# Performance work log

Measured on AMD Instinct MI355X. Metric: run time of the kernel, lower is better.

The kernel has to match this reference:

```python
import jax, jax.numpy as jnp
import numpy as np

B, C, T = 64, 1, 262144
NUM_BANDS = 6
# (min, max) for each of the 18 normalized control params: 6 bands x (gain_dB, cutoff_Hz, Q)
PARAM_RANGES = np.array([
    [-24.0, 24.0], [20.0, 200.0], [0.1, 10.0],      # low shelf
    [-24.0, 24.0], [200.0, 2000.0], [0.1, 10.0],    # band 1
    [-24.0, 24.0], [200.0, 2000.0], [0.1, 10.0],    # band 2
    [-24.0, 24.0], [2000.0, 8000.0], [0.1, 10.0],   # band 3
    [-24.0, 24.0], [4000.0, 12000.0], [0.1, 10.0],  # band 4
    [-24.0, 24.0], [4000.0, 12000.0], [0.1, 10.0],  # high shelf
], dtype=np.float32)
FILTER_TYPES = ["low_shelf", "peaking", "peaking", "peaking", "peaking", "high_shelf"]


def biquad_coeffs(gain_dB, cutoff, q, sr, ftype):
    # Audio-EQ-cookbook biquad coefficients; all inputs shape (B,)
    A = 10.0 ** (gain_dB / 40.0)
    w0 = 2.0 * jnp.pi * (cutoff / sr)
    alpha = jnp.sin(w0) / (2.0 * q)
    c = jnp.cos(w0)
    sA = jnp.sqrt(A)
    if ftype == "low_shelf":
        b0 = A * ((A + 1) - (A - 1) * c + 2 * sA * alpha)
        b1 = 2 * A * ((A - 1) - (A + 1) * c)
        b2 = A * ((A + 1) - (A - 1) * c - 2 * sA * alpha)
        a0 = (A + 1) + (A - 1) * c + 2 * sA * alpha
        a1 = -2 * ((A - 1) + (A + 1) * c)
        a2 = (A + 1) + (A - 1) * c - 2 * sA * alpha
    elif ftype == "high_shelf":
        b0 = A * ((A + 1) + (A - 1) * c + 2 * sA * alpha)
        b1 = -2 * A * ((A - 1) + (A + 1) * c)
        b2 = A * ((A + 1) + (A - 1) * c - 2 * sA * alpha)
        a0 = (A + 1) - (A - 1) * c + 2 * sA * alpha
        a1 = 2 * ((A - 1) - (A + 1) * c)
        a2 = (A + 1) - (A - 1) * c - 2 * sA * alpha
    else:  # peaking
        b0 = 1 + alpha * A
        b1 = -2 * c
        b2 = 1 - alpha * A
        a0 = 1 + alpha / A
        a1 = -2 * c
        a2 = 1 - alpha / A
    bcoef = jnp.stack([b0, b1, b2], axis=-1) / a0[..., None]  # (B, 3)
    acoef = jnp.stack([a0, a1, a2], axis=-1) / a0[..., None]  # (B, 3)
    return bcoef, acoef


def cascade_biquads(x, bcoefs, acoefs):
    # x: (N, T); bcoefs/acoefs: (6, N, 3). Fused cascade of 6 biquads,
    # direct form II transposed, single scan over time.
    def step(state, xt):  # state: (6, N, 2); xt: (N,)
        v = xt
        new_states = []
        for k in range(NUM_BANDS):
            bk, ak = bcoefs[k], acoefs[k]
            s1, s2 = state[k, :, 0], state[k, :, 1]
            y = bk[:, 0] * v + s1
            ns1 = bk[:, 1] * v - ak[:, 1] * y + s2
            ns2 = bk[:, 2] * v - ak[:, 2] * y
            new_states.append(jnp.stack([ns1, ns2], axis=-1))
            v = y
        return jnp.stack(new_states, axis=0), v
    init = jnp.zeros((NUM_BANDS, x.shape[0], 2), dtype=x.dtype)
    _, y = jax.lax.scan(step, init, x.T)  # y: (T, N)
    return y.T


def setup_inputs() -> dict:
    key = jax.random.key(0)
    k1, k2, k3 = jax.random.split(key, 3)
    x = jax.random.normal(k1, (B, C, T), dtype=jnp.float32) * 0.1
    p = jax.random.normal(k2, (B, 22), dtype=jnp.float32)
    W = jax.random.normal(k3, (18, 22), dtype=jnp.float32) * (1.0 / np.sqrt(22.0))
    b = jnp.zeros((18,), dtype=jnp.float32)
    return {"x": x, "p": p, "W": W, "b": b, "sample_rate": 24000}


def reference(x, p, W, b, sample_rate):
    bs, chs, s = x.shape
    sr = jnp.float32(sample_rate)
    # control path: linear + sigmoid -> 18 normalized params in [0, 1]
    pn = jax.nn.sigmoid(p @ W.T + b)  # (bs, 18)
    lo = jnp.asarray(PARAM_RANGES[:, 0])
    hi = jnp.asarray(PARAM_RANGES[:, 1])
    params = pn * (hi - lo) + lo  # denormalized, (bs, 18)
    bcoefs, acoefs = [], []
    for k, ftype in enumerate(FILTER_TYPES):
        g, f, q = params[:, 3 * k], params[:, 3 * k + 1], params[:, 3 * k + 2]
        bk, ak = biquad_coeffs(g, f, q, sr, ftype)
        bcoefs.append(bk)
        acoefs.append(ak)
    bcoefs = jnp.stack(bcoefs, axis=0)  # (6, bs, 3)
    acoefs = jnp.stack(acoefs, axis=0)
    # share each item's EQ across its channels
    bcoefs = jnp.repeat(bcoefs, chs, axis=1)  # (6, bs*chs, 3)
    acoefs = jnp.repeat(acoefs, chs, axis=1)
    y = cascade_biquads(x.reshape(bs * chs, s), bcoefs, acoefs)
    return y.reshape(bs, chs, s)
```

## Files before the change

### kernel.cpp

```cpp
#include <hip/hip_runtime.h>
#include <math.h>

#define NB    64
#define NT    262144
#define CH    64
#define NCK   (NT/CH)
#define NBANDS 6

#define COEF_OFF 0
#define MAT_OFF  4096
#define T_OFF    (MAT_OFF + NB*1728)
#define V_OFF    (T_OFF + NB*64*12)

struct Coef { float b0, b1, b2, a1, a2; };

__device__ __forceinline__ float rfl(float x) {
  return __int_as_float(__builtin_amdgcn_readfirstlane(__float_as_int(x)));
}

__device__ __forceinline__ float cascade_step(float v, float s[12], const Coef cf[NBANDS]) {
#pragma unroll
  for (int k = 0; k < NBANDS; ++k) {
    float s1 = s[2*k], s2 = s[2*k+1];
    float y   = fmaf(cf[k].b0, v, s1);
    float ns1 = fmaf(cf[k].b1, v, fmaf(-cf[k].a1, y, s2));
    float ns2 = fmaf(cf[k].b2, v, -cf[k].a2 * y);
    s[2*k]   = ns1;
    s[2*k+1] = ns2;
    v = y;
  }
  return v;
}

__device__ __forceinline__ void load_coefs(const float* ws, int batch, Coef cf[NBANDS]) {
  const float* c = ws + COEF_OFF + batch*30;
#pragma unroll
  for (int k = 0; k < NBANDS; ++k) {
    cf[k].b0 = rfl(c[5*k+0]); cf[k].b1 = rfl(c[5*k+1]); cf[k].b2 = rfl(c[5*k+2]);
    cf[k].a1 = rfl(c[5*k+3]); cf[k].a2 = rfl(c[5*k+4]);
  }
}

__global__ __launch_bounds__(64) void k_prep(const float* __restrict__ p, const float* __restrict__ W,
                                             const float* __restrict__ bias, const int* __restrict__ srp,
                                             float* __restrict__ ws) {
  __shared__ float prmS[18];
  __shared__ float cfS[30];
  __shared__ float M0[144], M1[144];
  int b = blockIdx.x, tid = threadIdx.x;
  const float lo[18] = {-24.f,20.f,0.1f,  -24.f,200.f,0.1f,  -24.f,200.f,0.1f,
                        -24.f,2000.f,0.1f, -24.f,4000.f,0.1f, -24.f,4000.f,0.1f};
  const float hi[18] = { 24.f,200.f,10.f,  24.f,2000.f,10.f,  24.f,2000.f,10.f,
                         24.f,8000.f,10.f, 24.f,12000.f,10.f, 24.f,12000.f,10.f};
  if (tid < 18) {
    float acc = bias[tid];
    for (int j = 0; j < 22; ++j) acc = fmaf(W[tid*22+j], p[b*22+j], acc);
    float sg = 1.f / (1.f + expf(-acc));
    prmS[tid] = sg * (hi[tid] - lo[tid]) + lo[tid];
  }
  __syncthreads();
  if (tid < 6) {
    int k = tid;
    float g = prmS[3*k], f = prmS[3*k+1], q = prmS[3*k+2];
    float sr = (float)srp[0];
    float A  = powf(10.f, g * (1.f/40.f));
    float w0 = 6.28318530717958647692f * (f / sr);
    float al = sinf(w0) / (2.f*q);
    float c  = cosf(w0);
    float sA = sqrtf(A);
    float b0,b1,b2,a0,a1,a2;
    if (k == 0) {
      b0 = A*((A+1.f) - (A-1.f)*c + 2.f*sA*al);
      b1 = 2.f*A*((A-1.f) - (A+1.f)*c);
      b2 = A*((A+1.f) - (A-1.f)*c - 2.f*sA*al);
      a0 = (A+1.f) + (A-1.f)*c + 2.f*sA*al;
      a1 = -2.f*((A-1.f) + (A+1.f)*c);
      a2 = (A+1.f) + (A-1.f)*c - 2.f*sA*al;
    } else if (k == 5) {
      b0 = A*((A+1.f) + (A-1.f)*c + 2.f*sA*al);
      b1 = -2.f*A*((A-1.f) + (A+1.f)*c);
      b2 = A*((A+1.f) + (A-1.f)*c - 2.f*sA*al);
      a0 = (A+1.f) - (A-1.f)*c + 2.f*sA*al;
      a1 = 2.f*((A-1.f) - (A+1.f)*c);
      a2 = (A+1.f) - (A-1.f)*c - 2.f*sA*al;
    } else {
      b0 = 1.f + al*A;
      b1 = -2.f*c;
      b2 = 1.f - al*A;
      a0 = 1.f + al/A;
      a1 = -2.f*c;
      a2 = 1.f - al/A;
    }
    float inv = 1.f/a0;
    float* cws = ws + COEF_OFF + b*30;
    cws[5*k+0] = cfS[5*k+0] = b0*inv;
    cws[5*k+1] = cfS[5*k+1] = b1*inv;
    cws[5*k+2] = cfS[5*k+2] = b2*inv;
    cws[5*k+3] = cfS[5*k+3] = a1*inv;
    cws[5*k+4] = cfS[5*k+4] = a2*inv;
  }
  __syncthreads();

  Coef cf[NBANDS];
#pragma unroll
  for (int k = 0; k < NBANDS; ++k) {
    cf[k].b0 = cfS[5*k+0]; cf[k].b1 = cfS[5*k+1]; cf[k].b2 = cfS[5*k+2];
    cf[k].a1 = cfS[5*k+3]; cf[k].a2 = cfS[5*k+4];
  }
  if (tid < 12) {
    float s[12];
#pragma unroll
    for (int r = 0; r < 12; ++r) s[r] = (r == tid) ? 1.f : 0.f;
    cascade_step(0.f, s, cf);
#pragma unroll
    for (int r = 0; r < 12; ++r) M0[r*12 + tid] = s[r];
  }
  __syncthreads();

  float w[12];
#pragma unroll
  for (int r = 0; r < 12; ++r) w[r] = 0.f;
  cascade_step(1.f, w, cf);
  int e63 = 63 - tid;

  float* S = M0; float* D = M1;
  float* mout = ws + MAT_OFF + (size_t)b*1728;
  for (int q = 0; q < 6; ++q) {
    if ((e63 >> q) & 1) {
      float t[12];
#pragma unroll
      for (int r = 0; r < 12; ++r) {
        float acc = 0.f;
#pragma unroll
        for (int k = 0; k < 12; ++k) acc = fmaf(S[r*12+k], w[k], acc);
        t[r] = acc;
      }
#pragma unroll
      for (int r = 0; r < 12; ++r) w[r] = t[r];
    }
    for (int e = tid; e < 144; e += 64) {
      int r = e/12, c = e%12;
      float acc = 0.f;
#pragma unroll
      for (int k = 0; k < 12; ++k) acc = fmaf(S[r*12+k], S[k*12+c], acc);
      D[e] = acc;
    }
    __syncthreads();
    float* t = S; S = D; D = t;
  }
  {
    float* vout = ws + V_OFF + (size_t)b*768;
#pragma unroll
    for (int r = 0; r < 12; ++r) vout[tid*12 + r] = w[r];
  }
  for (int e = tid; e < 144; e += 64) mout[e] = S[e];
  for (int l = 1; l < 12; ++l) {
    for (int e = tid; e < 144; e += 64) {
      int r = e/12, c = e%12;
      float acc = 0.f;
#pragma unroll
      for (int k = 0; k < 12; ++k) acc = fmaf(S[r*12+k], S[k*12+c], acc);
      D[e] = acc;
    }
    __syncthreads();
    float* t = S; S = D; D = t;
    for (int e = tid; e < 144; e += 64) mout[l*144 + e] = S[e];
  }
}

__global__ __launch_bounds__(256, 4) void k_totals(const float* __restrict__ x,
                                                   float* __restrict__ ws) {
  __shared__ float KM[6][144];
  int tid = threadIdx.x, wib = tid >> 6, lane = tid & 63;
  int gw = blockIdx.x*4 + wib;
  int batch = gw >> 6, wv = gw & 63;
  int batch_b = blockIdx.x >> 4;

  const float* mb = ws + MAT_OFF + (size_t)batch_b*1728;
  for (int e = tid; e < 864; e += 256) KM[e/144][e%144] = mb[e];
  __syncthreads();

  const float4* x4 = (const float4*)x;
  size_t gbase4 = (size_t)batch*65536 + (size_t)wv*1024 + (size_t)lane*16;
  const float* Vb = ws + V_OFF + (size_t)batch_b*768;

  float4 xv[16];
#pragma unroll
  for (int k = 0; k < 16; ++k) xv[k] = x4[gbase4 + k];

  float s[12];
#pragma unroll
  for (int r = 0; r < 12; ++r) s[r] = 0.f;
#pragma unroll
  for (int k = 0; k < 16; ++k) {
    const float* vr = Vb + k*48;
#pragma unroll
    for (int r = 0; r < 12; ++r) {
      float acc = s[r];
      acc = fmaf(vr[r],      xv[k].x, acc);
      acc = fmaf(vr[12 + r], xv[k].y, acc);
      acc = fmaf(vr[24 + r], xv[k].z, acc);
      acc = fmaf(vr[36 + r], xv[k].w, acc);
      s[r] = acc;
    }
  }

#pragma unroll
  for (int l = 0; l < 6; ++l) {
    const int pd = 1 << l;
    float nb[12];
#pragma unroll
    for (int r = 0; r < 12; ++r) nb[r] = __shfl_up(s[r], pd);
    if (lane >= pd) {
#pragma unroll
      for (int r = 0; r < 12; ++r) {
        float acc = s[r];
#pragma unroll
        for (int c = 0; c < 12; ++c) acc = fmaf(KM[l][r*12+c], nb[c], acc);
        s[r] = acc;
      }
    }
  }

  if (lane == 63) {
    float4* tp = (float4*)(ws + T_OFF + ((size_t)batch*64 + wv)*12);
    tp[0] = make_float4(s[0], s[1], s[2],  s[3]);
    tp[1] = make_float4(s[4], s[5], s[6],  s[7]);
    tp[2] = make_float4(s[8], s[9], s[10], s[11]);
  }
}

__global__ __launch_bounds__(256, 4) void k_replay(const float* __restrict__ x,
                                                   const float* __restrict__ ws,
                                                   float* __restrict__ out) {
  __shared__ float KM[12][144];
  __shared__ float4 sbuf[4][256];
  int tid = threadIdx.x, wib = tid >> 6, lane = tid & 63;
  int gw = blockIdx.x*4 + wib;
  int batch = gw >> 6, wv = gw & 63;
  int batch_b = blockIdx.x >> 4;

  const float* mb = ws + MAT_OFF + (size_t)batch_b*1728;
  for (int e = tid; e < 1728; e += 256) KM[e/144][e%144] = mb[e];

  Coef cf[NBANDS];
  load_coefs(ws, batch, cf);
  __syncthreads();

  const float4* x4 = (const float4*)x;
  float4* out4 = (float4*)out;
  size_t wbase4 = (size_t)batch*65536 + (size_t)wv*1024;
  size_t gbase4 = wbase4 + (size_t)lane*16;
  const float* Vb = ws + V_OFF + (size_t)batch_b*768;

  float4 xv[16];
#pragma unroll
  for (int k = 0; k < 16; ++k) xv[k] = x4[gbase4 + k];

  float s[12];
#pragma unroll
  for (int r = 0; r < 12; ++r) s[r] = 0.f;
#pragma unroll
  for (int k = 0; k < 16; ++k) {
    const float* vr = Vb + k*48;
#pragma unroll
    for (int r = 0; r < 12; ++r) {
      float acc = s[r];
      acc = fmaf(vr[r],      xv[k].x, acc);
      acc = fmaf(vr[12 + r], xv[k].y, acc);
      acc = fmaf(vr[24 + r], xv[k].z, acc);
      acc = fmaf(vr[36 + r], xv[k].w, acc);
      s[r] = acc;
    }
  }

#pragma unroll
  for (int l = 0; l < 6; ++l) {
    const int pd = 1 << l;
    float nb[12];
#pragma unroll
    for (int r = 0; r < 12; ++r) nb[r] = __shfl_up(s[r], pd);
    if (lane >= pd) {
#pragma unroll
      for (int r = 0; r < 12; ++r) {
        float acc = s[r];
#pragma unroll
        for (int c = 0; c < 12; ++c) acc = fmaf(KM[l][r*12+c], nb[c], acc);
        s[r] = acc;
      }
    }
  }

  float ex[12];
#pragma unroll
  for (int r = 0; r < 12; ++r) ex[r] = __shfl_up(s[r], 1);
  if (lane == 0) {
#pragma unroll
    for (int r = 0; r < 12; ++r) ex[r] = 0.f;
  }

  const float4* tp = (const float4*)(ws + T_OFF + ((size_t)batch*64 + lane)*12);
  float4 t0 = tp[0], t1 = tp[1], t2 = tp[2];
  float sc[12] = {t0.x,t0.y,t0.z,t0.w, t1.x,t1.y,t1.z,t1.w, t2.x,t2.y,t2.z,t2.w};
#pragma unroll
  for (int l = 0; l < 6; ++l) {
    const int pd = 1 << l;
    float nb[12];
#pragma unroll
    for (int r = 0; r < 12; ++r) nb[r] = __shfl_up(sc[r], pd);
    if (lane >= pd) {
#pragma unroll
      for (int r = 0; r < 12; ++r) {
        float acc = sc[r];
#pragma unroll
        for (int c = 0; c < 12; ++c) acc = fmaf(KM[6+l][r*12+c], nb[c], acc);
        sc[r] = acc;
      }
    }
  }

  int bsrc = (wv == 0) ? 0 : (wv - 1);
  float pre[12];
#pragma unroll
  for (int r = 0; r < 12; ++r) pre[r] = __shfl(sc[r], bsrc);
  if (wv == 0) {
#pragma unroll
    for (int r = 0; r < 12; ++r) pre[r] = 0.f;
  }

  float R[12];
#pragma unroll
  for (int r = 0; r < 12; ++r) R[r] = pre[r];
#pragma unroll
  for (int l = 0; l < 6; ++l) {
    float t[12];
#pragma unroll
    for (int r = 0; r < 12; ++r) {
      float acc = 0.f;
#pragma unroll
      for (int c = 0; c < 12; ++c) acc = fmaf(KM[l][r*12+c], R[c], acc);
      t[r] = acc;
    }
    bool sel = (lane >> l) & 1;
#pragma unroll
    for (int r = 0; r < 12; ++r) R[r] = sel ? t[r] : R[r];
  }

  float st[12];
#pragma unroll
  for (int r = 0; r < 12; ++r) st[r] = ex[r] + R[r];

  int r2 = lane >> 2, c2 = lane & 3;
  float4* bp = sbuf[wib];
#pragma unroll
  for (int q = 0; q < 4; ++q) {
#pragma unroll
    for (int t = 0; t < 4; ++t) {
      float4 xvv = xv[q*4 + t];
      float4 yv;
      yv.x = cascade_step(xvv.x, st, cf);
      yv.y = cascade_step(xvv.y, st, cf);
      yv.z = cascade_step(xvv.z, st, cf);
      yv.w = cascade_step(xvv.w, st, cf);
      bp[t*64 + lane] = yv;
    }
    asm volatile("s_waitcnt lgkmcnt(0)" ::: "memory");
#pragma unroll
    for (int j = 0; j < 4; ++j) {
      float4 w = bp[c2*64 + j*16 + r2];
      out4[wbase4 + (size_t)(j*16 + r2)*16 + q*4 + c2] = w;
    }
    asm volatile("s_waitcnt lgkmcnt(0)" ::: "memory");
  }
}

extern "C" void kernel_launch(void* const* d_in, const int* in_sizes, int n_in,
                              void* d_out, int out_size, void* d_ws, size_t ws_size,
                              hipStream_t stream) {
  const float* x    = (const float*)d_in[0];
  const float* p    = (const float*)d_in[1];
  const float* W    = (const float*)d_in[2];
  const float* bias = (const float*)d_in[3];
  const int*   sr   = (const int*)d_in[4];
  float* ws  = (float*)d_ws;
  float* out = (float*)d_out;

  int passBlocks = (NB * NCK) / 256;
  hipLaunchKernelGGL(k_prep,   dim3(NB),         dim3(64),  0, stream, p, W, bias, sr, ws);
  hipLaunchKernelGGL(k_totals, dim3(passBlocks), dim3(256), 0, stream, x, ws);
  hipLaunchKernelGGL(k_replay, dim3(passBlocks), dim3(256), 0, stream, x, ws, out);
}
```

Baseline: 111.8 us.

## Fuse totals and replay passes into one single-pass decoupled-lookback scan kernel

Replaces the two-pass scheme (a totals kernel, then a replay kernel that re-reads x) with one kernel. Each block takes an atomic ticket, computes its segment aggregate, publishes it with a release flag, and waits on the preceding segments' flags before combining them with precomputed matrix powers. This removes one full read of the input and one kernel launch. In exchange it adds spin-waiting on flags, extra matrix-power precompute in k_prep, more shared memory per block, and a lower occupancy bound.

After: 164.5 us. 1.47x slower.

```diff
diff --git a/kernel.cpp b/kernel.cpp
--- a/kernel.cpp
+++ b/kernel.cpp
@@ -3,14 +3,17 @@
 
 #define NB    64
 #define NT    262144
-#define CH    64
-#define NCK   (NT/CH)
 #define NBANDS 6
+#define SEGS  16
+#define SEGLEN 16384
 
 #define COEF_OFF 0
 #define MAT_OFF  4096
-#define T_OFF    (MAT_OFF + NB*1728)
-#define V_OFF    (T_OFF + NB*64*12)
+#define V_OFF    (MAT_OFF + NB*1728)
+#define PW_OFF   (V_OFF + NB*768)
+#define AGG_OFF  (PW_OFF + NB*2304)
+#define FLAG_OFF (AGG_OFF + NB*192)
+#define TICKET_OFF (FLAG_OFF + NB*16)
 
 struct Coef { float b0, b1, b2, a1, a2; };
 
@@ -46,8 +49,12 @@
                                              float* __restrict__ ws) {
   __shared__ float prmS[18];
   __shared__ float cfS[30];
-  __shared__ float M0[144], M1[144];
+  __shared__ float M0[144], M1[144], M2[144];
   int b = blockIdx.x, tid = threadIdx.x;
+
+  if (tid < SEGS) ((int*)ws)[FLAG_OFF + b*SEGS + tid] = 0;
+  if (b == 0 && tid == 0) ((int*)ws)[TICKET_OFF] = 0;
+
   const float lo[18] = {-24.f,20.f,0.1f,  -24.f,200.f,0.1f,  -24.f,200.f,0.1f,
                         -24.f,2000.f,0.1f, -24.f,4000.f,0.1f, -24.f,4000.f,0.1f};
   const float hi[18] = { 24.f,200.f,10.f,  24.f,2000.f,10.f,  24.f,2000.f,10.f,
@@ -166,27 +173,63 @@
     float* t = S; S = D; D = t;
     for (int e = tid; e < 144; e += 64) mout[l*144 + e] = S[e];
   }
-}
-
-__global__ __launch_bounds__(256, 4) void k_totals(const float* __restrict__ x,
-                                                   float* __restrict__ ws) {
-  __shared__ float KM[6][144];
-  int tid = threadIdx.x, wib = tid >> 6, lane = tid & 63;
-  int gw = blockIdx.x*4 + wib;
-  int batch = gw >> 6, wv = gw & 63;
-  int batch_b = blockIdx.x >> 4;
-
-  const float* mb = ws + MAT_OFF + (size_t)batch_b*1728;
-  for (int e = tid; e < 864; e += 256) KM[e/144][e%144] = mb[e];
-  __syncthreads();
+
+  __syncthreads();
+  for (int e = tid; e < 144; e += 64) M0[e] = mout[8*144 + e];
+  for (int e = tid; e < 144; e += 64) M1[e] = (e/12 == e%12) ? 1.f : 0.f;
+  __syncthreads();
+  float* Pc = M1; float* Pd = M2;
+  float* pout = ws + PW_OFF + (size_t)b*2304;
+  for (int e = tid; e < 144; e += 64) pout[e] = Pc[e];
+  for (int k = 1; k < 16; ++k) {
+    for (int e = tid; e < 144; e += 64) {
+      int r = e/12, c = e%12;
+      float acc = 0.f;
+#pragma unroll
+      for (int j = 0; j < 12; ++j) acc = fmaf(Pc[r*12+j], M0[j*12+c], acc);
+      Pd[e] = acc;
+    }
+    __syncthreads();
+    float* t = Pc; Pc = Pd; Pd = t;
+    for (int e = tid; e < 144; e += 64) pout[k*144 + e] = Pc[e];
+  }
+}
+
+__global__ __launch_bounds__(256, 2) void k_scan(const float* __restrict__ x,
+                                                 float* __restrict__ ws,
+                                                 float* __restrict__ out) {
+  __shared__ float KM[8][144];
+  __shared__ float PS[16][144];
+  __shared__ float Tsh[4][12];
+  __shared__ float S0sh[12];
+  __shared__ float4 buf[4][256];
+  __shared__ int vbidS;
+
+  int tid = threadIdx.x, w = tid >> 6, lane = tid & 63;
+
+  if (tid == 0) vbidS = atomicAdd((int*)ws + TICKET_OFF, 1);
+  __syncthreads();
+  int vbid = vbidS;
+  int batch = vbid >> 4, seg = vbid & (SEGS-1);
 
   const float4* x4 = (const float4*)x;
-  size_t gbase4 = (size_t)batch*65536 + (size_t)wv*1024 + (size_t)lane*16;
-  const float* Vb = ws + V_OFF + (size_t)batch_b*768;
+  float4* out4 = (float4*)out;
+  size_t wbase4 = (size_t)batch*65536 + (size_t)seg*4096 + (size_t)w*1024;
+  size_t gbase4 = wbase4 + (size_t)lane*16;
+  const float* Vb = ws + V_OFF + (size_t)batch*768;
 
   float4 xv[16];
 #pragma unroll
   for (int k = 0; k < 16; ++k) xv[k] = x4[gbase4 + k];
+
+  const float* mb = ws + MAT_OFF + (size_t)batch*1728;
+  for (int e = tid; e < 1152; e += 256) KM[e/144][e%144] = mb[e];
+  const float* pb = ws + PW_OFF + (size_t)batch*2304;
+  for (int e = tid; e < 2304; e += 256) PS[e/144][e%144] = pb[e];
+
+  Coef cf[NBANDS];
+  load_coefs(ws, batch, cf);
+  __syncthreads();
 
   float s[12];
 #pragma unroll
@@ -222,75 +265,6 @@
     }
   }
 
-  if (lane == 63) {
-    float4* tp = (float4*)(ws + T_OFF + ((size_t)batch*64 + wv)*12);
-    tp[0] = make_float4(s[0], s[1], s[2],  s[3]);
-    tp[1] = make_float4(s[4], s[5], s[6],  s[7]);
-    tp[2] = make_float4(s[8], s[9], s[10], s[11]);
-  }
-}
-
-__global__ __launch_bounds__(256, 4) void k_replay(const float* __restrict__ x,
-                                                   const float* __restrict__ ws,
-                                                   float* __restrict__ out) {
-  __shared__ float KM[12][144];
-  __shared__ float4 sbuf[4][256];
-  int tid = threadIdx.x, wib = tid >> 6, lane = tid & 63;
-  int gw = blockIdx.x*4 + wib;
-  int batch = gw >> 6, wv = gw & 63;
-  int batch_b = blockIdx.x >> 4;
-
-  const float* mb = ws + MAT_OFF + (size_t)batch_b*1728;
-  for (int e = tid; e < 1728; e += 256) KM[e/144][e%144] = mb[e];
-
-  Coef cf[NBANDS];
-  load_coefs(ws, batch, cf);
-  __syncthreads();
-
-  const float4* x4 = (const float4*)x;
-  float4* out4 = (float4*)out;
-  size_t wbase4 = (size_t)batch*65536 + (size_t)wv*1024;
-  size_t gbase4 = wbase4 + (size_t)lane*16;
-  const float* Vb = ws + V_OFF + (size_t)batch_b*768;
-
-  float4 xv[16];
-#pragma unroll
-  for (int k = 0; k < 16; ++k) xv[k] = x4[gbase4 + k];
-
-  float s[12];
-#pragma unroll
-  for (int r = 0; r < 12; ++r) s[r] = 0.f;
-#pragma unroll
-  for (int k = 0; k < 16; ++k) {
-    const float* vr = Vb + k*48;
-#pragma unroll
-    for (int r = 0; r < 12; ++r) {
-      float acc = s[r];
-      acc = fmaf(vr[r],      xv[k].x, acc);
-      acc = fmaf(vr[12 + r], xv[k].y, acc);
-      acc = fmaf(vr[24 + r], xv[k].z, acc);
-      acc = fmaf(vr[36 + r], xv[k].w, acc);
-      s[r] = acc;
-    }
-  }
-
-#pragma unroll
-  for (int l = 0; l < 6; ++l) {
-    const int pd = 1 << l;
-    float nb[12];
-#pragma unroll
-    for (int r = 0; r < 12; ++r) nb[r] = __shfl_up(s[r], pd);
-    if (lane >= pd) {
-#pragma unroll
-      for (int r = 0; r < 12; ++r) {
-        float acc = s[r];
-#pragma unroll
-        for (int c = 0; c < 12; ++c) acc = fmaf(KM[l][r*12+c], nb[c], acc);
-        s[r] = acc;
-      }
-    }
-  }
-
   float ex[12];
 #pragma unroll
   for (int r = 0; r < 12; ++r) ex[r] = __shfl_up(s[r], 1);
@@ -298,39 +272,118 @@
 #pragma unroll
     for (int r = 0; r < 12; ++r) ex[r] = 0.f;
   }
-
-  const float4* tp = (const float4*)(ws + T_OFF + ((size_t)batch*64 + lane)*12);
-  float4 t0 = tp[0], t1 = tp[1], t2 = tp[2];
-  float sc[12] = {t0.x,t0.y,t0.z,t0.w, t1.x,t1.y,t1.z,t1.w, t2.x,t2.y,t2.z,t2.w};
-#pragma unroll
-  for (int l = 0; l < 6; ++l) {
-    const int pd = 1 << l;
-    float nb[12];
-#pragma unroll
-    for (int r = 0; r < 12; ++r) nb[r] = __shfl_up(sc[r], pd);
-    if (lane >= pd) {
+  if (lane == 63) {
+#pragma unroll
+    for (int r = 0; r < 12; ++r) Tsh[w][r] = s[r];
+  }
+  __syncthreads();
+
+  float Q[12];
+#pragma unroll
+  for (int r = 0; r < 12; ++r) Q[r] = 0.f;
+  if (w > 0) {
+#pragma unroll
+    for (int r = 0; r < 12; ++r) Q[r] = Tsh[0][r];
+    for (int j = 1; j < w; ++j) {
+      float t[12];
 #pragma unroll
       for (int r = 0; r < 12; ++r) {
-        float acc = sc[r];
-#pragma unroll
-        for (int c = 0; c < 12; ++c) acc = fmaf(KM[6+l][r*12+c], nb[c], acc);
-        sc[r] = acc;
-      }
-    }
-  }
-
-  int bsrc = (wv == 0) ? 0 : (wv - 1);
-  float pre[12];
-#pragma unroll
-  for (int r = 0; r < 12; ++r) pre[r] = __shfl(sc[r], bsrc);
-  if (wv == 0) {
-#pragma unroll
-    for (int r = 0; r < 12; ++r) pre[r] = 0.f;
-  }
-
+        float acc = Tsh[j][r];
+#pragma unroll
+        for (int c = 0; c < 12; ++c) acc = fmaf(KM[6][r*12+c], Q[c], acc);
+        t[r] = acc;
+      }
+#pragma unroll
+      for (int r = 0; r < 12; ++r) Q[r] = t[r];
+    }
+  }
+
+  int* flags = (int*)ws + FLAG_OFF + batch*SEGS;
+  float* aggs = ws + AGG_OFF + (size_t)batch*192;
+  if (w == 0) {
+    float BT[12];
+#pragma unroll
+    for (int r = 0; r < 12; ++r) BT[r] = Tsh[0][r];
+    for (int j = 1; j < 4; ++j) {
+      float t[12];
+#pragma unroll
+      for (int r = 0; r < 12; ++r) {
+        float acc = Tsh[j][r];
+#pragma unroll
+        for (int c = 0; c < 12; ++c) acc = fmaf(KM[6][r*12+c], BT[c], acc);
+        t[r] = acc;
+      }
+#pragma unroll
+      for (int r = 0; r < 12; ++r) BT[r] = t[r];
+    }
+    if (lane == 0) {
+#pragma unroll
+      for (int r = 0; r < 12; ++r)
+        __hip_atomic_store(&aggs[seg*12 + r], BT[r], __ATOMIC_RELAXED, __HIP_MEMORY_SCOPE_AGENT);
+      __hip_atomic_store(&flags[seg], 1, __ATOMIC_RELEASE, __HIP_MEMORY_SCOPE_AGENT);
+    }
+    float Y[12];
+#pragma unroll
+    for (int r = 0; r < 12; ++r) Y[r] = 0.f;
+    if (lane < seg) {
+      int j = seg - 1 - lane;
+      while (__hip_atomic_load(&flags[j], __ATOMIC_ACQUIRE, __HIP_MEMORY_SCOPE_AGENT) == 0) {
+        __builtin_amdgcn_s_sleep(1);
+      }
+      float ag[12];
+#pragma unroll
+      for (int r = 0; r < 12; ++r)
+        ag[r] = __hip_atomic_load(&aggs[j*12 + r], __ATOMIC_RELAXED, __HIP_MEMORY_SCOPE_AGENT);
+#pragma unroll
+      for (int r = 0; r < 12; ++r) {
+        float acc = 0.f;
+#pragma unroll
+        for (int c = 0; c < 12; ++c) acc = fmaf(PS[lane][r*12+c], ag[c], acc);
+        Y[r] = acc;
+      }
+    }
+#pragma unroll
+    for (int o = 1; o < 16; o <<= 1) {
+#pragma unroll
+      for (int r = 0; r < 12; ++r) Y[r] += __shfl_xor(Y[r], o);
+    }
+    if (lane == 0) {
+#pragma unroll
+      for (int r = 0; r < 12; ++r) S0sh[r] = Y[r];
+    }
+  }
+  __syncthreads();
+
+  float V[12];
+#pragma unroll
+  for (int r = 0; r < 12; ++r) V[r] = S0sh[r];
+  if (w & 1) {
+    float t[12];
+#pragma unroll
+    for (int r = 0; r < 12; ++r) {
+      float acc = 0.f;
+#pragma unroll
+      for (int c = 0; c < 12; ++c) acc = fmaf(KM[6][r*12+c], V[c], acc);
+      t[r] = acc;
+    }
+#pragma unroll
+    for (int r = 0; r < 12; ++r) V[r] = t[r];
+  }
+  if (w & 2) {
+    float t[12];
+#pragma unroll
+    for (int r = 0; r < 12; ++r) {
+      float acc = 0.f;
+#pragma unroll
+      for (int c = 0; c < 12; ++c) acc = fmaf(KM[7][r*12+c], V[c], acc);
+      t[r] = acc;
+    }
+#pragma unroll
+    for (int r = 0; r < 12; ++r) V[r] = t[r];
+  }
   float R[12];
 #pragma unroll
-  for (int r = 0; r < 12; ++r) R[r] = pre[r];
+  for (int r = 0; r < 12; ++r) R[r] = Q[r] + V[r];
 #pragma unroll
   for (int l = 0; l < 6; ++l) {
     float t[12];
@@ -345,13 +398,12 @@
 #pragma unroll
     for (int r = 0; r < 12; ++r) R[r] = sel ? t[r] : R[r];
   }
-
   float st[12];
 #pragma unroll
   for (int r = 0; r < 12; ++r) st[r] = ex[r] + R[r];
 
   int r2 = lane >> 2, c2 = lane & 3;
-  float4* bp = sbuf[wib];
+  float4* bp = buf[w];
 #pragma unroll
   for (int q = 0; q < 4; ++q) {
 #pragma unroll
@@ -367,8 +419,8 @@
     asm volatile("s_waitcnt lgkmcnt(0)" ::: "memory");
 #pragma unroll
     for (int j = 0; j < 4; ++j) {
-      float4 w = bp[c2*64 + j*16 + r2];
-      out4[wbase4 + (size_t)(j*16 + r2)*16 + q*4 + c2] = w;
+      float4 wq = bp[c2*64 + j*16 + r2];
+      out4[wbase4 + (size_t)(j*16 + r2)*16 + q*4 + c2] = wq;
     }
     asm volatile("s_waitcnt lgkmcnt(0)" ::: "memory");
   }
@@ -385,8 +437,6 @@
   float* ws  = (float*)d_ws;
   float* out = (float*)d_out;
 
-  int passBlocks = (NB * NCK) / 256;
-  hipLaunchKernelGGL(k_prep,   dim3(NB),         dim3(64),  0, stream, p, W, bias, sr, ws);
-  hipLaunchKernelGGL(k_totals, dim3(passBlocks), dim3(256), 0, stream, x, ws);
-  hipLaunchKernelGGL(k_replay, dim3(passBlocks), dim3(256), 0, stream, x, ws, out);
-}
+  hipLaunchKernelGGL(k_prep, dim3(NB),      dim3(64),  0, stream, p, W, bias, sr, ws);
+  hipLaunchKernelGGL(k_scan, dim3(NB*SEGS), dim3(256), 0, stream, x, ws, out);
+}
```
